# Kernel tuning notes

Measured on AMD Instinct MI355X. Metric: run time of the kernel, lower is better.

Reference implementation:

```python
import jax, jax.numpy as jnp
import numpy as np

B, L, D, H, DEPTH, K = 16, 2048, 256, 8, 2, 7
HD = D // H
SCALE = HD ** -0.5


def _ln(x, g, b, eps=1e-5):
    m = x.mean(-1, keepdims=True)
    v = ((x - m) ** 2).mean(-1, keepdims=True)
    return (x - m) * jax.lax.rsqrt(v + eps) * g + b


def _nat_attn(x, qkv_w, qkv_b, proj_w, proj_b):
    # Neighborhood attention 1D: window of K tokens centered on each token,
    # clamped at sequence edges (NATTEN semantics, dilation=1).
    b, l, d = x.shape
    qkv = (x @ qkv_w + qkv_b).reshape(b, l, 3, H, HD).transpose(2, 0, 3, 1, 4)  # [3,B,H,L,hd]
    q, k, v = qkv[0] * SCALE, qkv[1], qkv[2]
    starts = jnp.clip(jnp.arange(l) - K // 2, 0, l - K)          # [L]
    idx = starts[:, None] + jnp.arange(K)                        # [L,K]
    kn = k[:, :, idx]                                            # [B,H,L,K,hd]
    vn = v[:, :, idx]
    attn = jax.nn.softmax(jnp.einsum('bhld,bhlkd->bhlk', q, kn), axis=-1)
    out = jnp.einsum('bhlk,bhlkd->bhld', attn, vn)               # [B,H,L,hd]
    out = out.transpose(0, 2, 1, 3).reshape(b, l, d)
    return out @ proj_w + proj_b


def _mlp(x, w1, b1, w2, b2):
    return jax.nn.gelu(x @ w1 + b1, approximate=False) @ w2 + b2


def setup_inputs() -> dict:
    key = jax.random.key(0)
    ks = jax.random.split(key, 8)
    s = 0.02
    return {
        'x': jax.random.normal(ks[0], (B, L, D), jnp.float32),
        'ln1_g': jnp.ones((DEPTH, D), jnp.float32),
        'ln1_b': jnp.zeros((DEPTH, D), jnp.float32),
        'qkv_w': jax.random.normal(ks[1], (DEPTH, D, 3 * D), jnp.float32) * s,
        'qkv_b': jnp.zeros((DEPTH, 3 * D), jnp.float32),
        'proj_w': jax.random.normal(ks[2], (DEPTH, D, D), jnp.float32) * s,
        'proj_b': jnp.zeros((DEPTH, D), jnp.float32),
        'ln2_g': jnp.ones((DEPTH, D), jnp.float32),
        'ln2_b': jnp.zeros((DEPTH, D), jnp.float32),
        'fc1_w': jax.random.normal(ks[3], (DEPTH, D, 4 * D), jnp.float32) * s,
        'fc1_b': jnp.zeros((DEPTH, 4 * D), jnp.float32),
        'fc2_w': jax.random.normal(ks[4], (DEPTH, 4 * D, D), jnp.float32) * s,
        'fc2_b': jnp.zeros((DEPTH, D), jnp.float32),
        'conv_w': jax.random.normal(ks[5], (2 * D, D, 3), jnp.float32) * s,  # OIH
        'dn_g': jnp.ones((2 * D,), jnp.float32),
        'dn_b': jnp.zeros((2 * D,), jnp.float32),
    }


def reference(x, ln1_g, ln1_b, qkv_w, qkv_b, proj_w, proj_b,
              ln2_g, ln2_b, fc1_w, fc1_b, fc2_w, fc2_b,
              conv_w, dn_g, dn_b):
    for i in range(DEPTH):
        h = _nat_attn(_ln(x, ln1_g[i], ln1_b[i]), qkv_w[i], qkv_b[i], proj_w[i], proj_b[i])
        x = x + h
        x = x + _mlp(_ln(x, ln2_g[i], ln2_b[i]), fc1_w[i], fc1_b[i], fc2_w[i], fc2_b[i])
    # ConvDownsampler: Conv1d(D, 2D, k=3, s=2, p=1, bias=False) + LayerNorm
    xc = x.transpose(0, 2, 1)  # [B,C,L]
    y = jax.lax.conv_general_dilated(xc, conv_w, window_strides=(2,),
                                     padding=[(1, 1)],
                                     dimension_numbers=('NCH', 'OIH', 'NCH'))
    y = y.transpose(0, 2, 1)   # [B, L//2, 2D]
    y = _ln(y, dn_g, dn_b)
    return (y, x)
```

## Files before the change

### kernel.cpp

```cpp
#include <hip/hip_runtime.h>

typedef unsigned short u16;
typedef __attribute__((ext_vector_type(8))) short bf16x8;
typedef __attribute__((ext_vector_type(4))) float f32x4;

__device__ __forceinline__ float bf2f(u16 u) { return __uint_as_float(((unsigned)u) << 16); }
__device__ __forceinline__ u16 f2bf(float f) {
    unsigned u = __float_as_uint(f);
    return (u16)((u + 0x7FFFu + ((u >> 16) & 1u)) >> 16);
}

__device__ __forceinline__ float gelu_fast(float v) {
    float u = v * (1.5957691216057308f + 0.07135481282700722f * v * v);
    return v * (1.f / (1.f + __expf(-u)));
}

__device__ __forceinline__ void load_lds16(const u16* g, u16* l) {
    __builtin_amdgcn_global_load_lds(
        (const __attribute__((address_space(1))) unsigned int*)g,
        (__attribute__((address_space(3))) unsigned int*)l,
        16, 0, 0);
}

template<int EPI>
__global__ __launch_bounds__(256) void gemm_kernel(
    const u16* __restrict__ A, const u16* __restrict__ Wt,
    const float* __restrict__ bias, const float* __restrict__ res,
    void* __restrict__ outp, int M, int N, int K)
{
    __shared__ __align__(16) u16 As[2][128 * 32];
    __shared__ __align__(16) u16 Bs[2][128 * 32];
    const int tid  = threadIdx.x;
    const int lane = tid & 63;
    const int wave = tid >> 6;
    const int row0 = blockIdx.x * 128;
    const int col0 = blockIdx.y * 128;
    const int wr = (wave >> 1) * 64;
    const int wc = (wave & 1) * 64;
    const int lr = lane & 15;
    const int q  = lane >> 4;

    f32x4 acc[4][4];
#pragma unroll
    for (int i = 0; i < 4; ++i)
#pragma unroll
        for (int j = 0; j < 4; ++j) acc[i][j] = (f32x4){0.f, 0.f, 0.f, 0.f};

    const int u0 = tid, u1 = tid + 256;
    const int r_u0 = u0 >> 2, r_u1 = u1 >> 2;
    const int c_u0 = (u0 & 3) ^ ((u0 >> 3) & 3);
    const int c_u1 = (u1 & 3) ^ ((u1 >> 3) & 3);
    const u16* agA0 = A  + (size_t)(row0 + r_u0) * K + c_u0 * 8;
    const u16* agA1 = A  + (size_t)(row0 + r_u1) * K + c_u1 * 8;
    const u16* bgB0 = Wt + (size_t)(col0 + r_u0) * K + c_u0 * 8;
    const u16* bgB1 = Wt + (size_t)(col0 + r_u1) * K + c_u1 * 8;

    const int nt = K >> 5;

    load_lds16(agA0, As[0] + u0 * 8);
    load_lds16(agA1, As[0] + u1 * 8);
    load_lds16(bgB0, Bs[0] + u0 * 8);
    load_lds16(bgB1, Bs[0] + u1 * 8);
    __syncthreads();

    for (int t = 0; t < nt; ++t) {
        if (t + 1 < nt) {
            const int p = (t + 1) & 1;
            const int k0 = (t + 1) << 5;
            load_lds16(agA0 + k0, As[p] + u0 * 8);
            load_lds16(agA1 + k0, As[p] + u1 * 8);
            load_lds16(bgB0 + k0, Bs[p] + u0 * 8);
            load_lds16(bgB1 + k0, Bs[p] + u1 * 8);
        }
        const u16* Ab = As[t & 1];
        const u16* Bb = Bs[t & 1];
        bf16x8 af[4], bfv[4];
#pragma unroll
        for (int i = 0; i < 4; ++i) {
            const int r = wr + i * 16 + lr;
            af[i] = *(const bf16x8*)(Ab + r * 32 + ((q ^ ((r >> 1) & 3)) * 8));
        }
#pragma unroll
        for (int j = 0; j < 4; ++j) {
            const int r = wc + j * 16 + lr;
            bfv[j] = *(const bf16x8*)(Bb + r * 32 + ((q ^ ((r >> 1) & 3)) * 8));
        }
#pragma unroll
        for (int i = 0; i < 4; ++i)
#pragma unroll
            for (int j = 0; j < 4; ++j)
                acc[i][j] = __builtin_amdgcn_mfma_f32_16x16x32_bf16(bfv[j], af[i], acc[i][j], 0, 0, 0);
        __syncthreads();
    }

    float4 bv[4];
#pragma unroll
    for (int j = 0; j < 4; ++j) {
        if (EPI == 3) { bv[j].x = bv[j].y = bv[j].z = bv[j].w = 0.f; }
        else          { bv[j] = *(const float4*)(bias + col0 + wc + j * 16 + q * 4); }
    }
#pragma unroll
    for (int i = 0; i < 4; ++i) {
        const int row = row0 + wr + i * 16 + lr;
#pragma unroll
        for (int j = 0; j < 4; ++j) {
            const int cb = col0 + wc + j * 16 + q * 4;
            float v0 = acc[i][j][0] + bv[j].x;
            float v1 = acc[i][j][1] + bv[j].y;
            float v2 = acc[i][j][2] + bv[j].z;
            float v3 = acc[i][j][3] + bv[j].w;
            if (EPI == 1) {
                const size_t o = (size_t)row * N + cb;
                const float4 rr = *(const float4*)(res + o);
                float4 ov;
                ov.x = v0 + rr.x; ov.y = v1 + rr.y; ov.z = v2 + rr.z; ov.w = v3 + rr.w;
                *(float4*)((float*)outp + o) = ov;
            } else {
                if (EPI == 2) {
                    v0 = gelu_fast(v0); v1 = gelu_fast(v1);
                    v2 = gelu_fast(v2); v3 = gelu_fast(v3);
                }
                ushort4 ov;
                ov.x = f2bf(v0); ov.y = f2bf(v1); ov.z = f2bf(v2); ov.w = f2bf(v3);
                *(ushort4*)((u16*)outp + (size_t)row * N + cb) = ov;
            }
        }
    }
}

__global__ __launch_bounds__(256) void ln_f2b_kernel(
    const float* __restrict__ x, const float* __restrict__ g,
    const float* __restrict__ be, u16* __restrict__ out)
{
    const int lane = threadIdx.x & 63;
    const int row  = blockIdx.x * 4 + (threadIdx.x >> 6);
    const float4 a = *(const float4*)(x + (size_t)row * 256 + lane * 4);
    float v[4] = {a.x, a.y, a.z, a.w};
    float s = v[0] + v[1] + v[2] + v[3];
#pragma unroll
    for (int m = 1; m < 64; m <<= 1) s += __shfl_xor(s, m);
    const float mean = s * (1.f / 256.f);
    float s2 = 0.f;
#pragma unroll
    for (int e = 0; e < 4; ++e) { float d = v[e] - mean; s2 += d * d; }
#pragma unroll
    for (int m = 1; m < 64; m <<= 1) s2 += __shfl_xor(s2, m);
    const float rstd = rsqrtf(s2 * (1.f / 256.f) + 1e-5f);
    const float4 gg = *(const float4*)(g + lane * 4);
    const float4 bb = *(const float4*)(be + lane * 4);
    ushort4 o;
    o.x = f2bf((v[0] - mean) * rstd * gg.x + bb.x);
    o.y = f2bf((v[1] - mean) * rstd * gg.y + bb.y);
    o.z = f2bf((v[2] - mean) * rstd * gg.z + bb.z);
    o.w = f2bf((v[3] - mean) * rstd * gg.w + bb.w);
    *(ushort4*)(out + (size_t)row * 256 + lane * 4) = o;
}

__global__ __launch_bounds__(256) void ln_b2f_kernel(
    const u16* __restrict__ x, const float* __restrict__ g,
    const float* __restrict__ be, float* __restrict__ out)
{
    const int lane = threadIdx.x & 63;
    const int row  = blockIdx.x * 4 + (threadIdx.x >> 6);
    const u16* xr = x + (size_t)row * 512 + lane * 8;
    float v[8];
#pragma unroll
    for (int e = 0; e < 8; e += 4) {
        ushort4 a = *(const ushort4*)(xr + e);
        v[e] = bf2f(a.x); v[e+1] = bf2f(a.y); v[e+2] = bf2f(a.z); v[e+3] = bf2f(a.w);
    }
    float s = 0.f;
#pragma unroll
    for (int e = 0; e < 8; ++e) s += v[e];
#pragma unroll
    for (int m = 1; m < 64; m <<= 1) s += __shfl_xor(s, m);
    const float mean = s * (1.f / 512.f);
    float s2 = 0.f;
#pragma unroll
    for (int e = 0; e < 8; ++e) { float d = v[e] - mean; s2 += d * d; }
#pragma unroll
    for (int m = 1; m < 64; m <<= 1) s2 += __shfl_xor(s2, m);
    const float rstd = rsqrtf(s2 * (1.f / 512.f) + 1e-5f);
    float* orow = out + (size_t)row * 512 + lane * 8;
#pragma unroll
    for (int e = 0; e < 8; e += 4) {
        float4 o;
        o.x = (v[e]   - mean) * rstd * g[lane*8+e]   + be[lane*8+e];
        o.y = (v[e+1] - mean) * rstd * g[lane*8+e+1] + be[lane*8+e+1];
        o.z = (v[e+2] - mean) * rstd * g[lane*8+e+2] + be[lane*8+e+2];
        o.w = (v[e+3] - mean) * rstd * g[lane*8+e+3] + be[lane*8+e+3];
        *(float4*)(orow + e) = o;
    }
}

__global__ __launch_bounds__(256) void attn_kernel(
    const u16* __restrict__ qkv, u16* __restrict__ out)
{
    const int lane  = threadIdx.x & 63;
    const int token = blockIdx.x * 4 + (threadIdx.x >> 6);
    const int b = token >> 11;
    const int l = token & 2047;
    const int h = lane >> 3;
    const int s = lane & 7;
    const int off = h * 32 + s * 4;

    ushort4 q4 = *(const ushort4*)(qkv + (size_t)token * 768 + off);
    const float scale = 0.17677669529663687f;
    float q0 = bf2f(q4.x), q1 = bf2f(q4.y), q2 = bf2f(q4.z), q3 = bf2f(q4.w);

    int start = l - 3;
    start = start < 0 ? 0 : (start > 2041 ? 2041 : start);
    const u16* kbase = qkv + ((size_t)(b << 11) + start) * 768 + 256 + off;

    float sc[7], vv[7][4];
#pragma unroll
    for (int j = 0; j < 7; ++j) {
        const u16* kp = kbase + (size_t)j * 768;
        ushort4 k4 = *(const ushort4*)kp;
        ushort4 v4 = *(const ushort4*)(kp + 256);
        float d = q0 * bf2f(k4.x) + q1 * bf2f(k4.y) + q2 * bf2f(k4.z) + q3 * bf2f(k4.w);
        d += __shfl_xor(d, 1); d += __shfl_xor(d, 2); d += __shfl_xor(d, 4);
        sc[j] = d * scale;
        vv[j][0] = bf2f(v4.x); vv[j][1] = bf2f(v4.y); vv[j][2] = bf2f(v4.z); vv[j][3] = bf2f(v4.w);
    }
    float mx = sc[0];
#pragma unroll
    for (int j = 1; j < 7; ++j) mx = fmaxf(mx, sc[j]);
    float p[7], sum = 0.f;
#pragma unroll
    for (int j = 0; j < 7; ++j) { p[j] = __expf(sc[j] - mx); sum += p[j]; }
    const float inv = 1.f / sum;
    float o0 = 0, o1 = 0, o2 = 0, o3 = 0;
#pragma unroll
    for (int j = 0; j < 7; ++j) {
        o0 += p[j] * vv[j][0]; o1 += p[j] * vv[j][1];
        o2 += p[j] * vv[j][2]; o3 += p[j] * vv[j][3];
    }
    ushort4 o;
    o.x = f2bf(o0 * inv); o.y = f2bf(o1 * inv); o.z = f2bf(o2 * inv); o.w = f2bf(o3 * inv);
    *(ushort4*)(out + (size_t)token * 256 + off) = o;
}

__global__ __launch_bounds__(256) void transpose_kernel(
    const float* __restrict__ in, u16* __restrict__ out, int K, int N)
{
    __shared__ float t[32][33];
    const int n0 = blockIdx.x * 32;
    const int k0 = blockIdx.y * 32;
    const int d  = blockIdx.z;
    const int tr = threadIdx.x >> 3;
    const int tc = (threadIdx.x & 7) * 4;
    const float4 a = *(const float4*)(in + ((size_t)d * K + k0 + tr) * N + n0 + tc);
    t[tc + 0][tr] = a.x; t[tc + 1][tr] = a.y; t[tc + 2][tr] = a.z; t[tc + 3][tr] = a.w;
    __syncthreads();
    ushort4 o;
    o.x = f2bf(t[tr][tc + 0]); o.y = f2bf(t[tr][tc + 1]);
    o.z = f2bf(t[tr][tc + 2]); o.w = f2bf(t[tr][tc + 3]);
    *(ushort4*)(out + ((size_t)d * N + n0 + tr) * K + k0 + tc) = o;
}

__global__ void convw_kernel(const float* __restrict__ in, u16* __restrict__ out)
{
    int idx = blockIdx.x * 256 + threadIdx.x;
    int r  = idx % 768;
    int co = idx / 768;
    int t  = r / 256;
    int ci = r % 256;
    out[idx] = f2bf(in[(size_t)co * 768 + (size_t)ci * 3 + t]);
}

__global__ __launch_bounds__(256) void im2col_kernel(
    const float* __restrict__ x, u16* __restrict__ x2, int r0)
{
    int idx = blockIdx.x * 256 + threadIdx.x;
    int c4  = idx & 63;
    int t   = (idx >> 6) % 3;
    int rl  = idx / 192;
    int row = r0 + rl;
    int b   = row >> 10;
    int lo  = row & 1023;
    int l   = 2 * lo + t - 1;
    ushort4 o = {0, 0, 0, 0};
    if (l >= 0 && l < 2048) {
        float4 val = *(const float4*)(x + ((size_t)(b << 11) + l) * 256 + c4 * 4);
        o.x = f2bf(val.x); o.y = f2bf(val.y); o.z = f2bf(val.z); o.w = f2bf(val.w);
    }
    *(ushort4*)(x2 + (size_t)rl * 768 + t * 256 + c4 * 4) = o;
}

extern "C" void kernel_launch(void* const* d_in, const int* in_sizes, int n_in,
                              void* d_out, int out_size, void* d_ws, size_t ws_size,
                              hipStream_t stream)
{
    const float* x_in   = (const float*)d_in[0];
    const float* ln1_g  = (const float*)d_in[1];
    const float* ln1_b  = (const float*)d_in[2];
    const float* qkv_w  = (const float*)d_in[3];
    const float* qkv_b  = (const float*)d_in[4];
    const float* proj_w = (const float*)d_in[5];
    const float* proj_b = (const float*)d_in[6];
    const float* ln2_g  = (const float*)d_in[7];
    const float* ln2_b  = (const float*)d_in[8];
    const float* fc1_w  = (const float*)d_in[9];
    const float* fc1_b  = (const float*)d_in[10];
    const float* fc2_w  = (const float*)d_in[11];
    const float* fc2_b  = (const float*)d_in[12];
    const float* conv_w = (const float*)d_in[13];
    const float* dn_g   = (const float*)d_in[14];
    const float* dn_b   = (const float*)d_in[15];

    float* xbuf = (float*)d_out + 8388608;
    u16*   xn   = (u16*)d_out;

    char* ws = (char*)d_ws;
    const size_t MB = 1024ull * 1024;
    u16* qkv_wt  = (u16*)ws;
    u16* proj_wt = qkv_wt  + 2 * 768 * 256;
    u16* fc1_wt  = proj_wt + 2 * 256 * 256;
    u16* fc2_wt  = fc1_wt  + 2 * 1024 * 256;
    u16* conv_wt = fc2_wt  + 2 * 256 * 1024;
    u16* S       = (u16*)(ws + 4 * MB);

    const size_t R = ws_size > 4 * MB ? ws_size - 4 * MB : 0;
    int nb = 16;    while (nb > 1 && (size_t)nb * 4 * MB > R) nb >>= 1;
    int Mf = 32768; while (Mf > 2048 && (size_t)Mf * 2048 > R) Mf >>= 1;
    int Mc = 16384; while (Mc > 2048 && (size_t)Mc * 2560 > R) Mc >>= 1;

    transpose_kernel<<<dim3(768 / 32, 256 / 32, 2), 256, 0, stream>>>(qkv_w,  qkv_wt,  256, 768);
    transpose_kernel<<<dim3(256 / 32, 256 / 32, 2), 256, 0, stream>>>(proj_w, proj_wt, 256, 256);
    transpose_kernel<<<dim3(1024 / 32, 256 / 32, 2), 256, 0, stream>>>(fc1_w, fc1_wt, 256, 1024);
    transpose_kernel<<<dim3(256 / 32, 1024 / 32, 2), 256, 0, stream>>>(fc2_w, fc2_wt, 1024, 256);
    convw_kernel<<<(512 * 768) / 256, 256, 0, stream>>>(conv_w, conv_wt);

    for (int layer = 0; layer < 2; ++layer) {
        const float* l1g = ln1_g + layer * 256;
        const float* l1b = ln1_b + layer * 256;
        const float* l2g = ln2_g + layer * 256;
        const float* l2b = ln2_b + layer * 256;
        const u16*   qwt = qkv_wt  + (size_t)layer * 768 * 256;
        const float* qb  = qkv_b   + layer * 768;
        const u16*   pwt = proj_wt + (size_t)layer * 256 * 256;
        const float* pb  = proj_b  + layer * 256;
        const u16*   f1w = fc1_wt  + (size_t)layer * 1024 * 256;
        const float* f1b = fc1_b   + layer * 1024;
        const u16*   f2w = fc2_wt  + (size_t)layer * 256 * 1024;
        const float* f2b = fc2_b   + layer * 256;

        const float* xsrc = (layer == 0) ? x_in : xbuf;

        ln_f2b_kernel<<<8192, 256, 0, stream>>>(xsrc, l1g, l1b, xn);
        {
            const int Mg = nb * 2048;
            u16* qkvc  = S;
            u16* atnoc = S + (size_t)Mg * 768;
            for (int g = 0; g < 16 / nb; ++g) {
                const size_t t0 = (size_t)g * Mg;
                gemm_kernel<0><<<dim3(Mg / 128, 6), 256, 0, stream>>>(
                    xn + t0 * 256, qwt, qb, nullptr, qkvc, Mg, 768, 256);
                attn_kernel<<<Mg / 4, 256, 0, stream>>>(qkvc, atnoc);
                gemm_kernel<1><<<dim3(Mg / 128, 2), 256, 0, stream>>>(
                    atnoc, pwt, pb, xsrc + t0 * 256, xbuf + t0 * 256, Mg, 256, 256);
            }
        }
        ln_f2b_kernel<<<8192, 256, 0, stream>>>(xbuf, l2g, l2b, xn);
        {
            u16* hbuf = S;
            for (int qq = 0; qq < 32768 / Mf; ++qq) {
                const size_t r0 = (size_t)qq * Mf;
                gemm_kernel<2><<<dim3(Mf / 128, 8), 256, 0, stream>>>(
                    xn + r0 * 256, f1w, f1b, nullptr, hbuf, Mf, 1024, 256);
                gemm_kernel<1><<<dim3(Mf / 128, 2), 256, 0, stream>>>(
                    hbuf, f2w, f2b, xbuf + r0 * 256, xbuf + r0 * 256, Mf, 256, 1024);
            }
        }
    }

    {
        u16* x2c = S;
        u16* ycc = S + (size_t)Mc * 768;
        for (int c = 0; c < 16384 / Mc; ++c) {
            const int r0 = c * Mc;
            im2col_kernel<<<3 * Mc / 4, 256, 0, stream>>>(xbuf, x2c, r0);
            gemm_kernel<3><<<dim3(Mc / 128, 4), 256, 0, stream>>>(
                x2c, conv_wt, nullptr, nullptr, ycc, Mc, 512, 768);
            ln_b2f_kernel<<<Mc / 4, 256, 0, stream>>>(
                ycc, dn_g, dn_b, (float*)d_out + (size_t)r0 * 512);
        }
    }
}
```

Measured before the change: 501.9 us.

## Triple-buffer GEMM LDS tiles with prefetch distance two and one barrier per step

Changes the GEMM main loop from double-buffered LDS staging to a three-buffer ring that prefetches two K-tiles ahead. It uses explicit s_waitcnt vmcnt counts so each step waits only for the current tile's direct-to-LDS loads, and it needs a single barrier per iteration instead of one after compute. The aim is to hide more global-load latency behind MFMA work. In exchange, LDS use per block rises from 32 KB to 48 KB, which may lower occupancy, and correctness now depends on the hand-set wait counts.

```diff
diff --git a/kernel.cpp b/kernel.cpp
--- a/kernel.cpp
+++ b/kernel.cpp
@@ -28,8 +28,8 @@
     const float* __restrict__ bias, const float* __restrict__ res,
     void* __restrict__ outp, int M, int N, int K)
 {
-    __shared__ __align__(16) u16 As[2][128 * 32];
-    __shared__ __align__(16) u16 Bs[2][128 * 32];
+    __shared__ __align__(16) u16 As[3][128 * 32];
+    __shared__ __align__(16) u16 Bs[3][128 * 32];
     const int tid  = threadIdx.x;
     const int lane = tid & 63;
     const int wave = tid >> 6;
@@ -57,23 +57,17 @@
 
     const int nt = K >> 5;
 
-    load_lds16(agA0, As[0] + u0 * 8);
-    load_lds16(agA1, As[0] + u1 * 8);
-    load_lds16(bgB0, Bs[0] + u0 * 8);
-    load_lds16(bgB1, Bs[0] + u1 * 8);
-    __syncthreads();
-
-    for (int t = 0; t < nt; ++t) {
-        if (t + 1 < nt) {
-            const int p = (t + 1) & 1;
-            const int k0 = (t + 1) << 5;
-            load_lds16(agA0 + k0, As[p] + u0 * 8);
-            load_lds16(agA1 + k0, As[p] + u1 * 8);
-            load_lds16(bgB0 + k0, Bs[p] + u0 * 8);
-            load_lds16(bgB1 + k0, Bs[p] + u1 * 8);
-        }
-        const u16* Ab = As[t & 1];
-        const u16* Bb = Bs[t & 1];
+    auto stage = [&](int b, int t) {
+        const int k0 = t << 5;
+        load_lds16(agA0 + k0, As[b] + u0 * 8);
+        load_lds16(agA1 + k0, As[b] + u1 * 8);
+        load_lds16(bgB0 + k0, Bs[b] + u0 * 8);
+        load_lds16(bgB1 + k0, Bs[b] + u1 * 8);
+    };
+
+    auto compute = [&](int b) {
+        const u16* Ab = As[b];
+        const u16* Bb = Bs[b];
         bf16x8 af[4], bfv[4];
 #pragma unroll
         for (int i = 0; i < 4; ++i) {
@@ -90,8 +84,28 @@
 #pragma unroll
             for (int j = 0; j < 4; ++j)
                 acc[i][j] = __builtin_amdgcn_mfma_f32_16x16x32_bf16(bfv[j], af[i], acc[i][j], 0, 0, 0);
-        __syncthreads();
-    }
+    };
+
+    stage(0, 0);
+    stage(1, 1);
+
+    int bc = 0;
+#pragma unroll 1
+    for (int t = 0; t < nt - 1; ++t) {
+        asm volatile("s_waitcnt vmcnt(4)" ::: "memory");
+        __builtin_amdgcn_s_barrier();
+        asm volatile("" ::: "memory");
+        if (t + 2 < nt) {
+            int bs = bc + 2; if (bs >= 3) bs -= 3;
+            stage(bs, t + 2);
+        }
+        compute(bc);
+        if (++bc == 3) bc = 0;
+    }
+    asm volatile("s_waitcnt vmcnt(0)" ::: "memory");
+    __builtin_amdgcn_s_barrier();
+    asm volatile("" ::: "memory");
+    compute(bc);
 
     float4 bv[4];
 #pragma unroll
```

New measurement: 499.5 us. About the same (-0.5%).

## Stage full-K weight slab in LDS and stream activations directly from global

Applied to the files above, without the earlier changes.

Replaces the double-buffered A/B LDS GEMM with a kernel that loads a 128x256 weight chunk into LDS (64 KB, XOR-swizzled) and reads activation fragments straight from global memory into registers, prefetching one k-step ahead. The grid is also transposed so blocks sharing a row tile launch adjacently, which helps L2 reuse of A. This removes the per-32-k sync and the LDS traffic for A. In exchange it uses much more LDS per block, which lowers occupancy, and A loads from global are not coalesced through LDS and have latency exposed across k-steps.

```diff
diff --git a/kernel.cpp b/kernel.cpp
--- a/kernel.cpp
+++ b/kernel.cpp
@@ -22,23 +22,23 @@
         16, 0, 0);
 }
 
-template<int EPI>
-__global__ __launch_bounds__(256) void gemm_kernel(
+template<int EPI, int NKC>
+__global__ __launch_bounds__(256) void gemm_rs(
     const u16* __restrict__ A, const u16* __restrict__ Wt,
     const float* __restrict__ bias, const float* __restrict__ res,
-    void* __restrict__ outp, int M, int N, int K)
-{
-    __shared__ __align__(16) u16 As[2][128 * 32];
-    __shared__ __align__(16) u16 Bs[2][128 * 32];
+    void* __restrict__ outp, int M, int N)
+{
+    __shared__ __align__(16) u16 Ws[128 * 256];
     const int tid  = threadIdx.x;
     const int lane = tid & 63;
     const int wave = tid >> 6;
-    const int row0 = blockIdx.x * 128;
-    const int col0 = blockIdx.y * 128;
+    const int col0 = blockIdx.x * 128;
+    const int row0 = blockIdx.y * 128;
     const int wr = (wave >> 1) * 64;
     const int wc = (wave & 1) * 64;
     const int lr = lane & 15;
     const int q  = lane >> 4;
+    const int K  = NKC * 256;
 
     f32x4 acc[4][4];
 #pragma unroll
@@ -46,51 +46,47 @@
 #pragma unroll
         for (int j = 0; j < 4; ++j) acc[i][j] = (f32x4){0.f, 0.f, 0.f, 0.f};
 
-    const int u0 = tid, u1 = tid + 256;
-    const int r_u0 = u0 >> 2, r_u1 = u1 >> 2;
-    const int c_u0 = (u0 & 3) ^ ((u0 >> 3) & 3);
-    const int c_u1 = (u1 & 3) ^ ((u1 >> 3) & 3);
-    const u16* agA0 = A  + (size_t)(row0 + r_u0) * K + c_u0 * 8;
-    const u16* agA1 = A  + (size_t)(row0 + r_u1) * K + c_u1 * 8;
-    const u16* bgB0 = Wt + (size_t)(col0 + r_u0) * K + c_u0 * 8;
-    const u16* bgB1 = Wt + (size_t)(col0 + r_u1) * K + c_u1 * 8;
-
-    const int nt = K >> 5;
-
-    load_lds16(agA0, As[0] + u0 * 8);
-    load_lds16(agA1, As[0] + u1 * 8);
-    load_lds16(bgB0, Bs[0] + u0 * 8);
-    load_lds16(bgB1, Bs[0] + u1 * 8);
-    __syncthreads();
-
-    for (int t = 0; t < nt; ++t) {
-        if (t + 1 < nt) {
-            const int p = (t + 1) & 1;
-            const int k0 = (t + 1) << 5;
-            load_lds16(agA0 + k0, As[p] + u0 * 8);
-            load_lds16(agA1 + k0, As[p] + u1 * 8);
-            load_lds16(bgB0 + k0, Bs[p] + u0 * 8);
-            load_lds16(bgB1 + k0, Bs[p] + u1 * 8);
-        }
-        const u16* Ab = As[t & 1];
-        const u16* Bb = Bs[t & 1];
-        bf16x8 af[4], bfv[4];
-#pragma unroll
-        for (int i = 0; i < 4; ++i) {
-            const int r = wr + i * 16 + lr;
-            af[i] = *(const bf16x8*)(Ab + r * 32 + ((q ^ ((r >> 1) & 3)) * 8));
-        }
-#pragma unroll
-        for (int j = 0; j < 4; ++j) {
-            const int r = wc + j * 16 + lr;
-            bfv[j] = *(const bf16x8*)(Bb + r * 32 + ((q ^ ((r >> 1) & 3)) * 8));
-        }
+    const u16* arow[4];
+#pragma unroll
+    for (int i = 0; i < 4; ++i)
+        arow[i] = A + (size_t)(row0 + wr + i * 16 + lr) * K + q * 8;
+
+    const int sch = (tid & 31) ^ ((tid >> 5) & 7);
+    const u16* wg = Wt + (size_t)(col0 + (tid >> 5)) * K + sch * 8;
+
+#pragma unroll 1
+    for (int kc = 0; kc < NKC; ++kc) {
+#pragma unroll
+        for (int s = 0; s < 16; ++s)
+            load_lds16(wg + (size_t)(s * 8) * K + kc * 256, Ws + (s * 256 + tid) * 8);
+        __syncthreads();
+
+        bf16x8 af[4], afn[4];
 #pragma unroll
         for (int i = 0; i < 4; ++i)
-#pragma unroll
-            for (int j = 0; j < 4; ++j)
-                acc[i][j] = __builtin_amdgcn_mfma_f32_16x16x32_bf16(bfv[j], af[i], acc[i][j], 0, 0, 0);
-        __syncthreads();
+            af[i] = *(const bf16x8*)(arow[i] + kc * 256);
+#pragma unroll
+        for (int kk = 0; kk < 8; ++kk) {
+            if (kk < 7) {
+#pragma unroll
+                for (int i = 0; i < 4; ++i)
+                    afn[i] = *(const bf16x8*)(arow[i] + kc * 256 + (kk + 1) * 32);
+            }
+            bf16x8 bfv[4];
+#pragma unroll
+            for (int j = 0; j < 4; ++j) {
+                const int r = wc + j * 16 + lr;
+                bfv[j] = *(const bf16x8*)(Ws + r * 256 + (((kk * 4 + q) ^ (r & 7)) * 8));
+            }
+#pragma unroll
+            for (int i = 0; i < 4; ++i)
+#pragma unroll
+                for (int j = 0; j < 4; ++j)
+                    acc[i][j] = __builtin_amdgcn_mfma_f32_16x16x32_bf16(bfv[j], af[i], acc[i][j], 0, 0, 0);
+#pragma unroll
+            for (int i = 0; i < 4; ++i) af[i] = afn[i];
+        }
+        if (NKC > 1 && kc + 1 < NKC) __syncthreads();
     }
 
     float4 bv[4];
@@ -355,11 +351,11 @@
             u16* atnoc = S + (size_t)Mg * 768;
             for (int g = 0; g < 16 / nb; ++g) {
                 const size_t t0 = (size_t)g * Mg;
-                gemm_kernel<0><<<dim3(Mg / 128, 6), 256, 0, stream>>>(
-                    xn + t0 * 256, qwt, qb, nullptr, qkvc, Mg, 768, 256);
+                gemm_rs<0, 1><<<dim3(6, Mg / 128), 256, 0, stream>>>(
+                    xn + t0 * 256, qwt, qb, nullptr, qkvc, Mg, 768);
                 attn_kernel<<<Mg / 4, 256, 0, stream>>>(qkvc, atnoc);
-                gemm_kernel<1><<<dim3(Mg / 128, 2), 256, 0, stream>>>(
-                    atnoc, pwt, pb, xsrc + t0 * 256, xbuf + t0 * 256, Mg, 256, 256);
+                gemm_rs<1, 1><<<dim3(2, Mg / 128), 256, 0, stream>>>(
+                    atnoc, pwt, pb, xsrc + t0 * 256, xbuf + t0 * 256, Mg, 256);
             }
         }
         ln_f2b_kernel<<<8192, 256, 0, stream>>>(xbuf, l2g, l2b, xn);
@@ -367,10 +363,10 @@
             u16* hbuf = S;
             for (int qq = 0; qq < 32768 / Mf; ++qq) {
                 const size_t r0 = (size_t)qq * Mf;
-                gemm_kernel<2><<<dim3(Mf / 128, 8), 256, 0, stream>>>(
-                    xn + r0 * 256, f1w, f1b, nullptr, hbuf, Mf, 1024, 256);
-                gemm_kernel<1><<<dim3(Mf / 128, 2), 256, 0, stream>>>(
-                    hbuf, f2w, f2b, xbuf + r0 * 256, xbuf + r0 * 256, Mf, 256, 1024);
+                gemm_rs<2, 1><<<dim3(8, Mf / 128), 256, 0, stream>>>(
+                    xn + r0 * 256, f1w, f1b, nullptr, hbuf, Mf, 1024);
+                gemm_rs<1, 4><<<dim3(2, Mf / 128), 256, 0, stream>>>(
+                    hbuf, f2w, f2b, xbuf + r0 * 256, xbuf + r0 * 256, Mf, 256);
             }
         }
     }
@@ -381,8 +377,8 @@
         for (int c = 0; c < 16384 / Mc; ++c) {
             const int r0 = c * Mc;
             im2col_kernel<<<3 * Mc / 4, 256, 0, stream>>>(xbuf, x2c, r0);
-            gemm_kernel<3><<<dim3(Mc / 128, 4), 256, 0, stream>>>(
-                x2c, conv_wt, nullptr, nullptr, ycc, Mc, 512, 768);
+            gemm_rs<3, 3><<<dim3(4, Mc / 128), 256, 0, stream>>>(
+                x2c, conv_wt, nullptr, nullptr, ycc, Mc, 512);
             ln_b2f_kernel<<<Mc / 4, 256, 0, stream>>>(
                 ycc, dn_g, dn_b, (float*)d_out + (size_t)r0 * 512);
         }
```

Result: slower. 605.2 us (+20.6%).
